# Performance work log

Measured on AMD Instinct MI355X. Metric: run time of the kernel, lower is better.

The kernel has to match this reference:

```python
import jax, jax.numpy as jnp
import numpy as np

N, D = 262144, 128

def setup_inputs() -> dict:
    key = jax.random.key(0)
    k1, k2, k3 = jax.random.split(key, 3)
    return {
        "anchor": jax.random.normal(k1, (N, D), dtype=jnp.float32),
        "positive": jax.random.normal(k2, (N, D), dtype=jnp.float32),
        "negative": jax.random.normal(k3, (N, D), dtype=jnp.float32),
        "alpha": 45,
    }

def reference(anchor, positive, negative, alpha):
    # alpha in degrees -> radians
    a = 2.0 * np.pi * alpha / 360.0
    t2 = np.tan(a) ** 2  # tan^2(alpha), python float constant
    # diag((anchor+positive) @ negative^T) == row-wise dot product; avoid NxN matmul
    apn = jnp.sum((anchor + positive) * negative, axis=-1, keepdims=True)  # [N,1]
    ap = jnp.sum(anchor * positive, axis=-1, keepdims=True)               # [N,1]
    f = 4.0 * t2 * apn - 2.0 * (1.0 + t2) * ap                            # [N,1]
    # torch.logsumexp(f, dim=0) on [N,1] -> [1]
    loss = jax.scipy.special.logsumexp(f, axis=0)
    return loss
```

## Files before the change

### kernel.cpp

```cpp
#include <hip/hip_runtime.h>
#include <math.h>

#define NROWS 262144
#define DDIM  128
#define GRID_BLOCKS 2048

__device__ inline void lse_merge(float& m, float& s, float m2, float s2) {
    float mm = fmaxf(m, m2);
    s = s * expf(m - mm) + s2 * expf(m2 - mm);
    m = mm;
}

__global__ __launch_bounds__(256) void angular_partial_kernel(
    const float* __restrict__ A, const float* __restrict__ P,
    const float* __restrict__ Ng, const int* __restrict__ alpha,
    float2* __restrict__ partials)
{
    double ar = M_PI * (double)alpha[0] / 180.0;
    double td = tan(ar);
    float c1 = (float)(4.0 * td * td);
    float c2 = (float)(2.0 * (1.0 + td * td));

    const int tid  = threadIdx.x;
    const int lane = tid & 63;
    const int waveInBlock = tid >> 6;
    const int half = lane >> 5;
    const int c4   = lane & 31;

    const float4* A4 = (const float4*)A;
    const float4* P4 = (const float4*)P;
    const float4* N4 = (const float4*)Ng;

    float m = -3.0e38f, s = 0.0f;

    const int wavesPerGrid = gridDim.x * 4;
    const int waveId = blockIdx.x * 4 + waveInBlock;

    for (int rp = waveId; rp < NROWS / 2; rp += wavesPerGrid) {
        int row = rp * 2 + half;
        int idx = row * 32 + c4;
        float4 av = A4[idx];
        float4 pv = P4[idx];
        float4 nv = N4[idx];

        float ap  = av.x * pv.x + av.y * pv.y + av.z * pv.z + av.w * pv.w;
        float apn = (av.x + pv.x) * nv.x + (av.y + pv.y) * nv.y
                  + (av.z + pv.z) * nv.z + (av.w + pv.w) * nv.w;

        #pragma unroll
        for (int off = 16; off; off >>= 1) {
            ap  += __shfl_xor(ap,  off, 32);
            apn += __shfl_xor(apn, off, 32);
        }

        if (c4 == 0) {
            float f = c1 * apn - c2 * ap;
            float mm = fmaxf(m, f);
            s = s * expf(m - mm) + expf(f - mm);
            m = mm;
        }
    }

    #pragma unroll
    for (int off = 32; off; off >>= 1) {
        float m2 = __shfl_xor(m, off, 64);
        float s2 = __shfl_xor(s, off, 64);
        lse_merge(m, s, m2, s2);
    }

    __shared__ float sm[4];
    __shared__ float ss[4];
    if (lane == 0) { sm[waveInBlock] = m; ss[waveInBlock] = s; }
    __syncthreads();

    if (tid == 0) {
        float M = sm[0], S = ss[0];
        #pragma unroll
        for (int w = 1; w < 4; w++) lse_merge(M, S, sm[w], ss[w]);
        partials[blockIdx.x] = make_float2(M, S);
    }
}

__global__ __launch_bounds__(256) void angular_finalize_kernel(
    const float2* __restrict__ partials, int nPart, float* __restrict__ out)
{
    const int tid  = threadIdx.x;
    const int lane = tid & 63;
    const int waveInBlock = tid >> 6;

    float m = -3.0e38f, s = 0.0f;
    for (int i = tid; i < nPart; i += 256) {
        float2 p = partials[i];
        lse_merge(m, s, p.x, p.y);
    }

    #pragma unroll
    for (int off = 32; off; off >>= 1) {
        float m2 = __shfl_xor(m, off, 64);
        float s2 = __shfl_xor(s, off, 64);
        lse_merge(m, s, m2, s2);
    }

    __shared__ float sm[4];
    __shared__ float ss[4];
    if (lane == 0) { sm[waveInBlock] = m; ss[waveInBlock] = s; }
    __syncthreads();

    if (tid == 0) {
        float M = sm[0], S = ss[0];
        #pragma unroll
        for (int w = 1; w < 4; w++) lse_merge(M, S, sm[w], ss[w]);
        out[0] = M + logf(S);
    }
}

extern "C" void kernel_launch(void* const* d_in, const int* in_sizes, int n_in,
                              void* d_out, int out_size, void* d_ws, size_t ws_size,
                              hipStream_t stream) {
    const float* A  = (const float*)d_in[0];
    const float* P  = (const float*)d_in[1];
    const float* Ng = (const float*)d_in[2];
    const int* alpha = (const int*)d_in[3];
    float* out = (float*)d_out;
    float2* partials = (float2*)d_ws;

    angular_partial_kernel<<<GRID_BLOCKS, 256, 0, stream>>>(A, P, Ng, alpha, partials);
    angular_finalize_kernel<<<1, 256, 0, stream>>>(partials, GRID_BLOCKS, out);
}
```

Before: 80.09 us.

## Combine dot products before reduction, unroll two row pairs, use fast exp

Folds the two row dot products into a single weighted value per lane before the cross-lane shuffle, which halves the shuffle count. The stride loop becomes a fixed 8-iteration loop that issues loads for two row pairs per iteration. Every lane now runs the LSE update without a lane-0 guard, so the final wave reduction needs only one xor-32 step. The double-precision tan is replaced by fast float sin/cos, and expf by __expf, which may slightly reduce accuracy.

```diff
diff --git a/kernel.cpp b/kernel.cpp
--- a/kernel.cpp
+++ b/kernel.cpp
@@ -2,12 +2,13 @@
 #include <math.h>
 
 #define NROWS 262144
-#define DDIM  128
 #define GRID_BLOCKS 2048
+#define WAVES_TOTAL (GRID_BLOCKS * 4)
+#define NPAIRS (NROWS / 2)
 
 __device__ inline void lse_merge(float& m, float& s, float m2, float s2) {
     float mm = fmaxf(m, m2);
-    s = s * expf(m - mm) + s2 * expf(m2 - mm);
+    s = s * __expf(m - mm) + s2 * __expf(m2 - mm);
     m = mm;
 }
 
@@ -16,10 +17,11 @@
     const float* __restrict__ Ng, const int* __restrict__ alpha,
     float2* __restrict__ partials)
 {
-    double ar = M_PI * (double)alpha[0] / 180.0;
-    double td = tan(ar);
-    float c1 = (float)(4.0 * td * td);
-    float c2 = (float)(2.0 * (1.0 + td * td));
+    float a  = 0.017453292519943295f * (float)alpha[0];
+    float t  = __sinf(a) / __cosf(a);
+    float t2 = t * t;
+    float c1 = 4.0f * t2;
+    float c2 = 2.0f * (1.0f + t2);
 
     const int tid  = threadIdx.x;
     const int lane = tid & 63;
@@ -33,38 +35,42 @@
 
     float m = -3.0e38f, s = 0.0f;
 
-    const int wavesPerGrid = gridDim.x * 4;
     const int waveId = blockIdx.x * 4 + waveInBlock;
 
-    for (int rp = waveId; rp < NROWS / 2; rp += wavesPerGrid) {
-        int row = rp * 2 + half;
-        int idx = row * 32 + c4;
-        float4 av = A4[idx];
-        float4 pv = P4[idx];
-        float4 nv = N4[idx];
+    #pragma unroll 1
+    for (int j = 0; j < 8; ++j) {
+        const int pA = waveId + (2 * j)     * WAVES_TOTAL;
+        const int pB = waveId + (2 * j + 1) * WAVES_TOTAL;
+        const int ia = (pA * 2 + half) * 32 + c4;
+        const int ib = (pB * 2 + half) * 32 + c4;
 
-        float ap  = av.x * pv.x + av.y * pv.y + av.z * pv.z + av.w * pv.w;
-        float apn = (av.x + pv.x) * nv.x + (av.y + pv.y) * nv.y
-                  + (av.z + pv.z) * nv.z + (av.w + pv.w) * nv.w;
+        float4 avA = A4[ia], pvA = P4[ia], nvA = N4[ia];
+        float4 avB = A4[ib], pvB = P4[ib], nvB = N4[ib];
+
+        float apA = avA.x * pvA.x + avA.y * pvA.y + avA.z * pvA.z + avA.w * pvA.w;
+        float anA = (avA.x + pvA.x) * nvA.x + (avA.y + pvA.y) * nvA.y
+                  + (avA.z + pvA.z) * nvA.z + (avA.w + pvA.w) * nvA.w;
+        float gA  = fmaf(-c2, apA, c1 * anA);
+
+        float apB = avB.x * pvB.x + avB.y * pvB.y + avB.z * pvB.z + avB.w * pvB.w;
+        float anB = (avB.x + pvB.x) * nvB.x + (avB.y + pvB.y) * nvB.y
+                  + (avB.z + pvB.z) * nvB.z + (avB.w + pvB.w) * nvB.w;
+        float gB  = fmaf(-c2, apB, c1 * anB);
 
         #pragma unroll
         for (int off = 16; off; off >>= 1) {
-            ap  += __shfl_xor(ap,  off, 32);
-            apn += __shfl_xor(apn, off, 32);
+            gA += __shfl_xor(gA, off, 32);
+            gB += __shfl_xor(gB, off, 32);
         }
 
-        if (c4 == 0) {
-            float f = c1 * apn - c2 * ap;
-            float mm = fmaxf(m, f);
-            s = s * expf(m - mm) + expf(f - mm);
-            m = mm;
-        }
+        float ml = fmaxf(gA, gB);
+        float sl = __expf(gA - ml) + __expf(gB - ml);
+        lse_merge(m, s, ml, sl);
     }
 
-    #pragma unroll
-    for (int off = 32; off; off >>= 1) {
-        float m2 = __shfl_xor(m, off, 64);
-        float s2 = __shfl_xor(s, off, 64);
+    {
+        float m2 = __shfl_xor(m, 32, 64);
+        float s2 = __shfl_xor(s, 32, 64);
         lse_merge(m, s, m2, s2);
     }
 
```

After: 77.03 us. 1.04x faster.
